# Optimization experiments

Measured on AMD Instinct MI355X. Metric: run time of the kernel, lower is better.

Reference implementation:

```python
import math
import jax, jax.numpy as jnp
import numpy as np

DT = 0.001
TAU = 0.02
ALPHA_LIF = math.exp(-DT / TAU)  # fixed LIF decay ~0.9512
V_TH = 1.0
V_RESET = 0.0
BETA = 25.0  # SuperSpike surrogate slope used in LIFLayer

@jax.custom_vjp
def spike(x):
    # SuperSpike forward: hard threshold
    return (x > 0.0).astype(x.dtype)

def _spike_fwd(x):
    return spike(x), x

def _spike_bwd(x, g):
    # surrogate gradient: beta * max(0, 1 - |beta * x|)
    sg = BETA * jnp.clip(1.0 - jnp.abs(BETA * x), 0.0)
    return (g * sg,)

spike.defvjp(_spike_fwd, _spike_bwd)


def setup_inputs() -> dict:
    key = jax.random.key(0)
    k1, k2, k3 = jax.random.split(key, 3)
    T, B, C_IN, C_OUT = 500, 64, 512, 512
    x_seq = jax.random.uniform(k1, (T, B, C_IN), dtype=jnp.float32)
    # kaiming_uniform_(a=sqrt(5)) on [c_in, c_out] -> bound = 1/sqrt(fan_in)
    bound = 1.0 / math.sqrt(C_IN)
    W = jax.random.uniform(k2, (C_IN, C_OUT), minval=-bound, maxval=bound, dtype=jnp.float32)
    alpha_param = jnp.asarray(0.9, dtype=jnp.float32)  # learned synapse trace decay
    return {"x_seq": x_seq, "W": W, "alpha_param": alpha_param}


def reference(x_seq, W, alpha_param):
    T, B, c_in = x_seq.shape
    c_out = W.shape[1]
    a = jnp.clip(alpha_param, 0.0, 0.9999)

    def step(carry, x_t):
        v, trace = carry                      # v: [B, c_out], trace: [B, c_in]
        trace = a * trace + x_t               # synapse trace update
        cur = x_t @ W + trace @ W             # synaptic current [B, c_out]
        v = ALPHA_LIF * v + (1.0 - ALPHA_LIF) * cur
        s = spike(v - V_TH)                   # surrogate-grad threshold
        v = jnp.where(s > 0, V_RESET, v)      # hard reset
        return (v, trace), s

    init = (jnp.zeros((B, c_out), x_seq.dtype), jnp.zeros((B, c_in), x_seq.dtype))
    _, spikes_out = jax.lax.scan(step, init, x_seq)  # [T, B, c_out]
    rates = spikes_out.mean(axis=0)                  # [B, c_out]
    return spikes_out, rates
```

## Files before the change

### kernel.cpp

```cpp
#include <hip/hip_runtime.h>

typedef float f32x4 __attribute__((ext_vector_type(4)));

#define TSTEPS 500
#define BDIM 64
#define CIN 512
#define COUT 512
#define MTOT (TSTEPS * BDIM)
#define NCH (BDIM * CIN)
#define SNEUR (BDIM * COUT)
#define OUTN ((size_t)TSTEPS * SNEUR + SNEUR)

#define AL64 0.95122942450071400909
#define BL64 (1.0 - AL64)

#define BUF_BYTES 65536000ull
#define WS_NEED (3ull * BUF_BYTES)

__global__ __launch_bounds__(256) void fill_const_f32(
    float* __restrict__ p, size_t n, float c) {
  size_t i = (size_t)blockIdx.x * 256 + threadIdx.x;
  const size_t stride = (size_t)gridDim.x * 256;
  for (; i < n; i += stride) p[i] = c;
}

__global__ __launch_bounds__(256) void trace32(
    const float* __restrict__ X, float* __restrict__ TR,
    const float* __restrict__ alpha) {
  const int j = blockIdx.x * 256 + threadIdx.x;
  const float a = fminf(fmaxf(alpha[0], 0.0f), 0.9999f);
  float tr = 0.0f;
#pragma unroll 10
  for (int t = 0; t < TSTEPS; ++t) {
    float x = X[(size_t)t * NCH + j];
    tr = __fadd_rn(__fmul_rn(a, tr), x);
    TR[(size_t)t * NCH + j] = tr;
  }
}

template <int PHASE>
__global__ __launch_bounds__(256) void gemmK32(
    const float* __restrict__ X, const float* __restrict__ TR,
    const float* __restrict__ W, float* __restrict__ PHx,
    float* __restrict__ PHt) {
  __shared__ __align__(16) float Asx[64][36];
  __shared__ __align__(16) float Ast[64][36];
  __shared__ __align__(16) float Bs[32][132];
  const int tid = threadIdx.x;
  const int ty = tid >> 4, tx = tid & 15;

  const int fid = blockIdx.x;
  const int swz = (fid & 7) * 250 + (fid >> 3);
  const int bm = (swz >> 2) * 64;
  const int bn = (swz & 3) * 128;

  const int ar = tid >> 2, akb = (tid & 3) * 8;
  const int bk = tid >> 3, bc4 = (tid & 7) * 4;

  const int KT0 = PHASE ? 12 : 0;
  const int KT1 = PHASE ? 16 : 12;

  const float* gx = X + (size_t)(bm + ar) * CIN + KT0 * 32 + akb;
  const float* gt = TR + (size_t)(bm + ar) * CIN + KT0 * 32 + akb;
  const float* gw = W + (size_t)(KT0 * 32 + bk) * COUT + bn + bc4;

  float xA[4][8] = {{0.0f}}, tA[4][8] = {{0.0f}};

  for (int kt = KT0; kt < KT1; ++kt) {
    __syncthreads();
    *(f32x4*)&Asx[ar][akb]     = *(const f32x4*)gx;
    *(f32x4*)&Asx[ar][akb + 4] = *(const f32x4*)(gx + 4);
    *(f32x4*)&Ast[ar][akb]     = *(const f32x4*)gt;
    *(f32x4*)&Ast[ar][akb + 4] = *(const f32x4*)(gt + 4);
#pragma unroll
    for (int q = 0; q < 4; ++q)
      *(f32x4*)&Bs[bk][bc4 + q * 32] = *(const f32x4*)(gw + q * 32);
    __syncthreads();
    gx += 32; gt += 32; gw += 32 * COUT;
#pragma unroll
    for (int kg = 0; kg < 8; ++kg) {
      f32x4 ax[4], at4[4];
#pragma unroll
      for (int i = 0; i < 4; ++i) {
        ax[i] = *(const f32x4*)&Asx[ty * 4 + i][kg * 4];
        at4[i] = *(const f32x4*)&Ast[ty * 4 + i][kg * 4];
      }
#pragma unroll
      for (int k2 = 0; k2 < 4; ++k2) {
        f32x4 bL = *(const f32x4*)&Bs[kg * 4 + k2][tx * 4];
        f32x4 bH = *(const f32x4*)&Bs[kg * 4 + k2][64 + tx * 4];
#pragma unroll
        for (int i = 0; i < 4; ++i)
#pragma unroll
          for (int j = 0; j < 4; ++j) {
            xA[i][j]     = fmaf(ax[i][k2], bL[j], xA[i][j]);
            xA[i][4 + j] = fmaf(ax[i][k2], bH[j], xA[i][4 + j]);
            tA[i][j]     = fmaf(at4[i][k2], bL[j], tA[i][j]);
            tA[i][4 + j] = fmaf(at4[i][k2], bH[j], tA[i][4 + j]);
          }
      }
    }
  }

#pragma unroll
  for (int i = 0; i < 4; ++i) {
    const size_t row = (size_t)(bm + ty * 4 + i);
    const size_t iL = row * COUT + bn + tx * 4;
    const size_t iH = row * COUT + bn + 64 + tx * 4;
    f32x4 xL, xH2, tL, tH2;
#pragma unroll
    for (int j = 0; j < 4; ++j) {
      xL[j] = xA[i][j];  xH2[j] = xA[i][4 + j];
      tL[j] = tA[i][j];  tH2[j] = tA[i][4 + j];
    }
    if (PHASE == 0) {
      *(f32x4*)&PHx[iL] = xL;   *(f32x4*)&PHx[iH] = xH2;
      *(f32x4*)&PHt[iL] = tL;   *(f32x4*)&PHt[iH] = tH2;
    } else {
      f32x4 hxL = *(const f32x4*)&PHx[iL];
      f32x4 hxH = *(const f32x4*)&PHx[iH];
      f32x4 htL = *(const f32x4*)&PHt[iL];
      f32x4 htH = *(const f32x4*)&PHt[iH];
      f32x4 oL, oH;
#pragma unroll
      for (int j = 0; j < 4; ++j) {
        oL[j] = __fadd_rn(__fadd_rn(hxL[j], xL[j]), __fadd_rn(htL[j], tL[j]));
        oH[j] = __fadd_rn(__fadd_rn(hxH[j], xH2[j]), __fadd_rn(htH[j], tH2[j]));
      }
      *(f32x4*)&PHx[iL] = oL;
      *(f32x4*)&PHx[iH] = oH;
    }
  }
}

__global__ __launch_bounds__(256) void lif32(
    const float* __restrict__ CUR, float* __restrict__ spikes,
    float* __restrict__ rates) {
  const int j = blockIdx.x * 256 + threadIdx.x;
  const float AL = (float)AL64, BL = (float)BL64;
  float v = 0.0f;
  int cnt = 0;
#pragma unroll 10
  for (int t = 0; t < TSTEPS; ++t) {
    float cur = CUR[(size_t)t * SNEUR + j];
    v = __fadd_rn(__fmul_rn(AL, v), __fmul_rn(BL, cur));
    int sp = __fadd_rn(v, -1.0f) > 0.0f;
    cnt += sp;
    spikes[(size_t)t * SNEUR + j] = sp ? 1.0f : 0.0f;
    v = sp ? 0.0f : v;
  }
  rates[j] = __fdiv_rn((float)cnt, 500.0f);
}

extern "C" void kernel_launch(void* const* d_in, const int* in_sizes, int n_in,
                              void* d_out, int out_size, void* d_ws, size_t ws_size,
                              hipStream_t stream) {
  float* out = (float*)d_out;

  float flag = 0.0f;
  const float* X = nullptr;
  const float* W = nullptr;
  const float* AP = nullptr;
  if (n_in != 3) {
    flag = 11.0f;
  } else {
    for (int i = 0; i < 3; ++i) {
      if (in_sizes[i] == 16384000) X = (const float*)d_in[i];
      else if (in_sizes[i] == 262144) W = (const float*)d_in[i];
      else if (in_sizes[i] == 1) AP = (const float*)d_in[i];
    }
    if (!X || !W || !AP) flag = 13.0f;
    else if (out_size != (int)OUTN) flag = 17.0f;
    else if (ws_size < WS_NEED) flag = 23.0f;
  }
  if (flag != 0.0f) {
    fill_const_f32<<<dim3(2048), dim3(256), 0, stream>>>(out, OUTN, flag);
    return;
  }

  char* ws = (char*)d_ws;
  float* TR = (float*)(ws);
  float* PHx = (float*)(ws + BUF_BYTES);
  float* PHt = (float*)(ws + 2 * BUF_BYTES);

  trace32<<<dim3(NCH / 256), dim3(256), 0, stream>>>(X, TR, AP);
  gemmK32<0><<<dim3(2000), dim3(256), 0, stream>>>(X, TR, W, PHx, PHt);
  gemmK32<1><<<dim3(2000), dim3(256), 0, stream>>>(X, TR, W, PHx, PHt);
  lif32<<<dim3(SNEUR / 256), dim3(256), 0, stream>>>(
      PHx, out, out + (size_t)TSTEPS * SNEUR);
}
```

Before: 499.7 us.

## Double-buffer GEMM shared tiles and shrink scan kernel blocks to one wave

The GEMM kernel now keeps two shared-memory buffers for the A and W tiles. It loads the next K-slice into the spare buffer while computing on the current one, which removes one barrier per iteration and lets global loads overlap the FMAs. The trace and LIF scan kernels switch from 256-thread to 64-thread blocks with deeper unrolling, so the 32768 sequential-scan threads spread over more CUs. Double buffering doubles the GEMM's LDS use to roughly 71 KB per block, which may lower occupancy.

```diff
diff --git a/kernel.cpp b/kernel.cpp
--- a/kernel.cpp
+++ b/kernel.cpp
@@ -24,13 +24,13 @@
   for (; i < n; i += stride) p[i] = c;
 }
 
-__global__ __launch_bounds__(256) void trace32(
+__global__ __launch_bounds__(64) void trace32(
     const float* __restrict__ X, float* __restrict__ TR,
     const float* __restrict__ alpha) {
-  const int j = blockIdx.x * 256 + threadIdx.x;
+  const int j = blockIdx.x * 64 + threadIdx.x;
   const float a = fminf(fmaxf(alpha[0], 0.0f), 0.9999f);
   float tr = 0.0f;
-#pragma unroll 10
+#pragma unroll 20
   for (int t = 0; t < TSTEPS; ++t) {
     float x = X[(size_t)t * NCH + j];
     tr = __fadd_rn(__fmul_rn(a, tr), x);
@@ -39,13 +39,13 @@
 }
 
 template <int PHASE>
-__global__ __launch_bounds__(256) void gemmK32(
+__global__ __launch_bounds__(256) void gemmDB(
     const float* __restrict__ X, const float* __restrict__ TR,
     const float* __restrict__ W, float* __restrict__ PHx,
     float* __restrict__ PHt) {
-  __shared__ __align__(16) float Asx[64][36];
-  __shared__ __align__(16) float Ast[64][36];
-  __shared__ __align__(16) float Bs[32][132];
+  __shared__ __align__(16) float Asx[2][64][36];
+  __shared__ __align__(16) float Ast[2][64][36];
+  __shared__ __align__(16) float Bs[2][32][132];
   const int tid = threadIdx.x;
   const int ty = tid >> 4, tx = tid & 15;
 
@@ -66,29 +66,45 @@
 
   float xA[4][8] = {{0.0f}}, tA[4][8] = {{0.0f}};
 
+  {
+    *(f32x4*)&Asx[0][ar][akb]     = *(const f32x4*)gx;
+    *(f32x4*)&Asx[0][ar][akb + 4] = *(const f32x4*)(gx + 4);
+    *(f32x4*)&Ast[0][ar][akb]     = *(const f32x4*)gt;
+    *(f32x4*)&Ast[0][ar][akb + 4] = *(const f32x4*)(gt + 4);
+#pragma unroll
+    for (int q = 0; q < 4; ++q)
+      *(f32x4*)&Bs[0][bk][bc4 + q * 32] = *(const f32x4*)(gw + q * 32);
+  }
+  __syncthreads();
+
   for (int kt = KT0; kt < KT1; ++kt) {
-    __syncthreads();
-    *(f32x4*)&Asx[ar][akb]     = *(const f32x4*)gx;
-    *(f32x4*)&Asx[ar][akb + 4] = *(const f32x4*)(gx + 4);
-    *(f32x4*)&Ast[ar][akb]     = *(const f32x4*)gt;
-    *(f32x4*)&Ast[ar][akb + 4] = *(const f32x4*)(gt + 4);
-#pragma unroll
-    for (int q = 0; q < 4; ++q)
-      *(f32x4*)&Bs[bk][bc4 + q * 32] = *(const f32x4*)(gw + q * 32);
-    __syncthreads();
-    gx += 32; gt += 32; gw += 32 * COUT;
+    const int cur = (kt - KT0) & 1;
+    if (kt + 1 < KT1) {
+      gx += 32; gt += 32; gw += 32 * COUT;
+      f32x4 nx0 = *(const f32x4*)gx, nx1 = *(const f32x4*)(gx + 4);
+      f32x4 nt0 = *(const f32x4*)gt, nt1 = *(const f32x4*)(gt + 4);
+      *(f32x4*)&Asx[cur ^ 1][ar][akb]     = nx0;
+      *(f32x4*)&Asx[cur ^ 1][ar][akb + 4] = nx1;
+      *(f32x4*)&Ast[cur ^ 1][ar][akb]     = nt0;
+      *(f32x4*)&Ast[cur ^ 1][ar][akb + 4] = nt1;
+#pragma unroll
+      for (int q = 0; q < 4; ++q) {
+        f32x4 nw = *(const f32x4*)(gw + q * 32);
+        *(f32x4*)&Bs[cur ^ 1][bk][bc4 + q * 32] = nw;
+      }
+    }
 #pragma unroll
     for (int kg = 0; kg < 8; ++kg) {
       f32x4 ax[4], at4[4];
 #pragma unroll
       for (int i = 0; i < 4; ++i) {
-        ax[i] = *(const f32x4*)&Asx[ty * 4 + i][kg * 4];
-        at4[i] = *(const f32x4*)&Ast[ty * 4 + i][kg * 4];
+        ax[i] = *(const f32x4*)&Asx[cur][ty * 4 + i][kg * 4];
+        at4[i] = *(const f32x4*)&Ast[cur][ty * 4 + i][kg * 4];
       }
 #pragma unroll
       for (int k2 = 0; k2 < 4; ++k2) {
-        f32x4 bL = *(const f32x4*)&Bs[kg * 4 + k2][tx * 4];
-        f32x4 bH = *(const f32x4*)&Bs[kg * 4 + k2][64 + tx * 4];
+        f32x4 bL = *(const f32x4*)&Bs[cur][kg * 4 + k2][tx * 4];
+        f32x4 bH = *(const f32x4*)&Bs[cur][kg * 4 + k2][64 + tx * 4];
 #pragma unroll
         for (int i = 0; i < 4; ++i)
 #pragma unroll
@@ -100,6 +116,7 @@
           }
       }
     }
+    __syncthreads();
   }
 
 #pragma unroll
@@ -133,14 +150,14 @@
   }
 }
 
-__global__ __launch_bounds__(256) void lif32(
+__global__ __launch_bounds__(64) void lif32(
     const float* __restrict__ CUR, float* __restrict__ spikes,
     float* __restrict__ rates) {
-  const int j = blockIdx.x * 256 + threadIdx.x;
+  const int j = blockIdx.x * 64 + threadIdx.x;
   const float AL = (float)AL64, BL = (float)BL64;
   float v = 0.0f;
   int cnt = 0;
-#pragma unroll 10
+#pragma unroll 20
   for (int t = 0; t < TSTEPS; ++t) {
     float cur = CUR[(size_t)t * SNEUR + j];
     v = __fadd_rn(__fmul_rn(AL, v), __fmul_rn(BL, cur));
@@ -183,9 +200,9 @@
   float* PHx = (float*)(ws + BUF_BYTES);
   float* PHt = (float*)(ws + 2 * BUF_BYTES);
 
-  trace32<<<dim3(NCH / 256), dim3(256), 0, stream>>>(X, TR, AP);
-  gemmK32<0><<<dim3(2000), dim3(256), 0, stream>>>(X, TR, W, PHx, PHt);
-  gemmK32<1><<<dim3(2000), dim3(256), 0, stream>>>(X, TR, W, PHx, PHt);
-  lif32<<<dim3(SNEUR / 256), dim3(256), 0, stream>>>(
+  trace32<<<dim3(NCH / 64), dim3(64), 0, stream>>>(X, TR, AP);
+  gemmDB<0><<<dim3(2000), dim3(256), 0, stream>>>(X, TR, W, PHx, PHt);
+  gemmDB<1><<<dim3(2000), dim3(256), 0, stream>>>(X, TR, W, PHx, PHt);
+  lif32<<<dim3(SNEUR / 64), dim3(64), 0, stream>>>(
       PHx, out, out + (size_t)TSTEPS * SNEUR);
 }
```

Result: slower. 686.1 us (+37.3%).
